# Kernel optimization log

Hardware: AMD Instinct MI355X
Metric: run time of the kernel (lower is better)

The kernel has to match this reference:

```python
import jax, jax.numpy as jnp
import numpy as np

D_MODEL = 1024
NUM_HEADS = 16
HEAD_DIM = D_MODEL // NUM_HEADS


def setup_inputs() -> dict:
    key = jax.random.key(0)
    ks = jax.random.split(key, 5)
    x = jax.random.normal(ks[0], (4, 2048, D_MODEL), dtype=jnp.float32)
    # nn.Linear params: weight [out, in], bias [out]
    s_qkv = 1.0 / np.sqrt(D_MODEL)
    W_qkv = jax.random.uniform(ks[1], (3 * D_MODEL, D_MODEL), jnp.float32, -s_qkv, s_qkv)
    b_qkv = jax.random.uniform(ks[2], (3 * D_MODEL,), jnp.float32, -s_qkv, s_qkv)
    W_proj = jax.random.uniform(ks[3], (D_MODEL, D_MODEL), jnp.float32, -s_qkv, s_qkv)
    b_proj = jax.random.uniform(ks[4], (D_MODEL,), jnp.float32, -s_qkv, s_qkv)
    return {"x": x, "W_qkv": W_qkv, "b_qkv": b_qkv, "W_proj": W_proj, "b_proj": b_proj}


def reference(x, W_qkv, b_qkv, W_proj, b_proj):
    B, S, D = x.shape
    H, Hd = NUM_HEADS, HEAD_DIM
    qkv = x @ W_qkv.T + b_qkv                      # [B,S,3D]
    qkv = qkv.reshape(B, S, 3, H, Hd)
    q = qkv[:, :, 0].transpose(0, 2, 1, 3)        # [B,H,S,Hd]
    k = qkv[:, :, 1].transpose(0, 2, 1, 3)
    v = qkv[:, :, 2].transpose(0, 2, 1, 3)
    scale = jnp.sqrt(jnp.asarray(Hd, x.dtype))
    attn = jnp.einsum('bhqd,bhkd->bhqk', q, k) / scale   # [B,H,S,S]
    attn = jax.nn.softmax(attn, axis=-1)
    out = jnp.einsum('bhqk,bhkd->bhqd', attn, v)         # [B,H,S,Hd]
    out = out.transpose(0, 2, 1, 3).reshape(B, S, D)
    return out @ W_proj.T + b_proj
```

## Files before the change

### kernel.cpp

```cpp
#include <hip/hip_runtime.h>
#include <stdint.h>

#define SEQ    2048
#define DMODEL 1024
#define NH     16
#define HD     64
#define BATCH  4
#define MTOT   (BATCH*SEQ)
#define NT2    (SEQ/128)

typedef __attribute__((ext_vector_type(8))) short bf16x8;
typedef __attribute__((ext_vector_type(4))) float f32x4;
typedef __attribute__((ext_vector_type(2))) unsigned int uint2v;

#define QSCALE (0.125f * 1.44269504088896f)

__device__ __forceinline__ unsigned short f2bf(float f) {
  union { float f; uint32_t u; } x; x.f = f;
  uint32_t u = x.u;
  u += 0x7FFFu + ((u >> 16) & 1u);
  return (unsigned short)(u >> 16);
}

__device__ __forceinline__ float exp2_fast(float x) {
#if __has_builtin(__builtin_amdgcn_exp2f)
  return __builtin_amdgcn_exp2f(x);
#else
  return __expf(x * 0.69314718056f);
#endif
}

__device__ __forceinline__ uint32_t cvt_pk_bf16(float lo, float hi) {
  uint32_t r;
  asm("v_cvt_pk_bf16_f32 %0, %1, %2" : "=v"(r) : "v"(lo), "v"(hi));
  return r;
}

__device__ __forceinline__ void swap32(uint32_t& x, uint32_t& y) {
#if __has_builtin(__builtin_amdgcn_permlane32_swap)
  uint2v r = __builtin_amdgcn_permlane32_swap(x, y, false, false);
  x = r[0]; y = r[1];
#else
  unsigned int xs = __shfl_xor((unsigned int)x, 32);
  unsigned int ys = __shfl_xor((unsigned int)y, 32);
  const bool lo = ((threadIdx.x & 63) & 32) == 0;
  x = lo ? x : (uint32_t)ys;
  y = lo ? (uint32_t)xs : y;
#endif
}

__device__ __forceinline__ void swap16(uint32_t& x, uint32_t& y) {
#if __has_builtin(__builtin_amdgcn_permlane16_swap)
  uint2v r = __builtin_amdgcn_permlane16_swap(x, y, false, false);
  x = r[0]; y = r[1];
#else
  unsigned int xs = __shfl_xor((unsigned int)x, 16);
  unsigned int ys = __shfl_xor((unsigned int)y, 16);
  const bool lo = ((threadIdx.x & 63) & 16) == 0;
  x = lo ? x : (uint32_t)ys;
  y = lo ? (uint32_t)xs : y;
#endif
}

__device__ __forceinline__ void gload_lds16(const ushort* g, ushort* l) {
  __builtin_amdgcn_global_load_lds(
      (const __attribute__((address_space(1))) uint32_t*)g,
      (__attribute__((address_space(3))) uint32_t*)l, 16, 0, 0);
}

__global__ __launch_bounds__(256) void cvt_kernel(const float* __restrict__ in,
                                                  ushort* __restrict__ out, int n4) {
  int i = blockIdx.x * 256 + threadIdx.x;
  if (i >= n4) return;
  float4 v = ((const float4*)in)[i];
  ushort4 o;
  o.x = f2bf(v.x); o.y = f2bf(v.y); o.z = f2bf(v.z); o.w = f2bf(v.w);
  ((ushort4*)out)[i] = o;
}

template<int MODE>
__global__ __launch_bounds__(256)
void gemm_nt(const ushort* __restrict__ A, const ushort* __restrict__ B,
             const float* __restrict__ bias, float* __restrict__ outf,
             ushort* __restrict__ qo, ushort* __restrict__ ko, ushort* __restrict__ vto,
             int M, int N, int K)
{
  __shared__ ushort lda[128 * 64];
  __shared__ ushort ldb[128 * 64];
  const int tid = threadIdx.x;
  const int w = tid >> 6, lane = tid & 63;
  const int l15 = lane & 15, lg = lane >> 4;

  const int Nb = gridDim.x, Mb = gridDim.y;
  const int flat = blockIdx.y * Nb + blockIdx.x;
  const int q8 = (Nb * Mb) >> 3;
  const int nf2 = (flat & 7) * q8 + (flat >> 3);
  const int row0 = (nf2 % Mb) * 128;
  const int col0 = (nf2 / Mb) * 128;

  const int wm = (w >> 1) * 64, wn = (w & 1) * 64;
  const int sr = lane >> 3;
  const int scb = (lane & 7) ^ sr;
  const int rswz = l15 & 7;

  f32x4 acc[4][4];
#pragma unroll
  for (int i = 0; i < 4; ++i)
#pragma unroll
    for (int j = 0; j < 4; ++j) acc[i][j] = (f32x4){0.f, 0.f, 0.f, 0.f};

  const ushort* Ablk = A + (size_t)row0 * K;
  const ushort* Bblk = B + (size_t)col0 * K;

  for (int kt = 0; kt < K; kt += 64) {
#pragma unroll
    for (int i = 0; i < 4; ++i) {
      const int is = w * 4 + i;
      gload_lds16(Ablk + (size_t)(is * 8 + sr) * K + kt + scb * 8, lda + is * 512);
      gload_lds16(Bblk + (size_t)(is * 8 + sr) * K + kt + scb * 8, ldb + is * 512);
    }
    __syncthreads();
#pragma unroll
    for (int kki = 0; kki < 2; ++kki) {
      bf16x8 af[4], bfr[4];
#pragma unroll
      for (int i = 0; i < 4; ++i)
        af[i] = *(const bf16x8*)&lda[(wm + i * 16 + l15) * 64 + ((kki * 4 + lg) ^ rswz) * 8];
#pragma unroll
      for (int j = 0; j < 4; ++j)
        bfr[j] = *(const bf16x8*)&ldb[(wn + j * 16 + l15) * 64 + ((kki * 4 + lg) ^ rswz) * 8];
#pragma unroll
      for (int i = 0; i < 4; ++i)
#pragma unroll
        for (int j = 0; j < 4; ++j)
          acc[i][j] = __builtin_amdgcn_mfma_f32_16x16x32_bf16(af[i], bfr[j], acc[i][j], 0, 0, 0);
    }
    __syncthreads();
  }

#pragma unroll
  for (int i = 0; i < 4; ++i)
#pragma unroll
    for (int j = 0; j < 4; ++j) {
      const int n = col0 + wn + j * 16 + l15;
      const int m0 = row0 + wm + i * 16 + lg * 4;
      const float bn = bias[n];
      if (MODE == 1) {
#pragma unroll
        for (int r = 0; r < 4; ++r)
          outf[(size_t)(m0 + r) * N + n] = acc[i][j][r] + bn;
      } else {
        const int d = n & 1023;
        const int hh = d >> 6, hd = d & 63;
        const int bb = m0 >> 11, ss0 = m0 & 2047;
        const int which = n >> 10;
        if (which == 2) {
          ushort4 pk;
          pk.x = f2bf(acc[i][j][0] + bn);
          pk.y = f2bf(acc[i][j][1] + bn);
          pk.z = f2bf(acc[i][j][2] + bn);
          pk.w = f2bf(acc[i][j][3] + bn);
          *(ushort4*)&vto[(((size_t)bb * NH + hh) * HD + hd) * SEQ + ss0] = pk;
        } else {
          const size_t idx = (((size_t)bb * NH + hh) * SEQ + ss0) * HD + hd;
#pragma unroll
          for (int r = 0; r < 4; ++r) {
            const float val = acc[i][j][r] + bn;
            if (which == 0) qo[idx + (size_t)r * HD] = f2bf(val * QSCALE);
            else            ko[idx + (size_t)r * HD] = f2bf(val);
          }
        }
      }
    }
}

__global__ __launch_bounds__(256, 2)
void attn_kernel(const ushort* __restrict__ Q, const ushort* __restrict__ Kg,
                 const ushort* __restrict__ Vtg, ushort* __restrict__ O)
{
  __shared__ ushort ldk[2][2][64 * 64];
  __shared__ ushort ldvt[2][2][64 * 64];

  const int tid = threadIdx.x;
  const int w = tid >> 6, lane = tid & 63;
  const int l15 = lane & 15, lg = lane >> 4;

  const int bid = blockIdx.x;
  const int c = bid & 7, j = bid >> 3;
  const int bh = c + 8 * (j >> 3);
  const int qt = j & 7;
  const int b = bh >> 4, h = bh & 15;

  const ushort* Qb = Q + (size_t)bh * SEQ * HD;
  const ushort* Kb = Kg + (size_t)bh * SEQ * HD;
  const ushort* Vtb = Vtg + (size_t)bh * HD * SEQ;

  const int srow = lane >> 3;
  const int scb = (lane & 7) ^ srow;
  const int rswz = l15 & 7;

  const int qr0 = qt * 256 + w * 64;
  bf16x8 qf[4][2];
#pragma unroll
  for (int mi = 0; mi < 4; ++mi)
#pragma unroll
    for (int dk = 0; dk < 2; ++dk)
      qf[mi][dk] = *(const bf16x8*)&Qb[(size_t)(qr0 + mi * 16 + l15) * HD + dk * 32 + lg * 8];

  bf16x8 ones;
#pragma unroll
  for (int i = 0; i < 8; ++i) ones[i] = (short)0x3F80;

  f32x4 acc_o[4][4];
  f32x4 acc_l[4];
#pragma unroll
  for (int mi = 0; mi < 4; ++mi) {
#pragma unroll
    for (int nf = 0; nf < 4; ++nf) acc_o[mi][nf] = (f32x4){0.f, 0.f, 0.f, 0.f};
    acc_l[mi] = (f32x4){0.f, 0.f, 0.f, 0.f};
  }

#define STAGE(bufi, grp) do {                                                                  \
    _Pragma("unroll")                                                                          \
    for (int s_ = 0; s_ < 2; ++s_) {                                                           \
      const int t_ = 2 * (grp) + s_;                                                           \
      const ushort* Ks_ = Kb + (size_t)t_ * 64 * HD;                                           \
      const ushort* Vs_ = Vtb + (size_t)t_ * 64;                                               \
      _Pragma("unroll")                                                                        \
      for (int i_ = 0; i_ < 2; ++i_) {                                                         \
        const int is_ = w * 2 + i_;                                                            \
        gload_lds16(Ks_ + (size_t)(is_ * 8 + srow) * HD + scb * 8, &ldk[bufi][s_][is_ * 512]); \
        gload_lds16(Vs_ + (size_t)(is_ * 8 + srow) * SEQ + scb * 8, &ldvt[bufi][s_][is_ * 512]);\
      }                                                                                        \
    }                                                                                          \
  } while (0)

  int cur = 0;
  STAGE(0, 0);
  __syncthreads();

  for (int g = 0; g < NT2; ++g) {
    if (g + 1 < NT2) STAGE(cur ^ 1, g + 1);

#pragma unroll
    for (int s = 0; s < 2; ++s) {
      f32x4 accs[4][4];
#pragma unroll
      for (int a = 0; a < 4; ++a)
#pragma unroll
        for (int mi = 0; mi < 4; ++mi) accs[a][mi] = (f32x4){0.f, 0.f, 0.f, 0.f};
#pragma unroll
      for (int dk = 0; dk < 2; ++dk) {
        bf16x8 kfr[4];
#pragma unroll
        for (int a = 0; a < 4; ++a)
          kfr[a] = *(const bf16x8*)&ldk[cur][s][(a * 16 + l15) * 64 + ((dk * 4 + lg) ^ rswz) * 8];
        __builtin_amdgcn_s_setprio(1);
#pragma unroll
        for (int a = 0; a < 4; ++a)
#pragma unroll
          for (int mi = 0; mi < 4; ++mi)
            accs[a][mi] = __builtin_amdgcn_mfma_f32_16x16x32_bf16(kfr[a], qf[mi][dk], accs[a][mi], 0, 0, 0);
        __builtin_amdgcn_s_setprio(0);
      }

#pragma unroll
      for (int mi = 0; mi < 4; ++mi)
#pragma unroll
        for (int a = 0; a < 4; ++a)
#pragma unroll
          for (int r = 0; r < 4; ++r)
            accs[a][mi][r] = exp2_fast(accs[a][mi][r]);

#pragma unroll
      for (int kk = 0; kk < 2; ++kk) {
        bf16x8 vv[4];
#pragma unroll
        for (int nf = 0; nf < 4; ++nf)
          vv[nf] = *(const bf16x8*)&ldvt[cur][s][(nf * 16 + l15) * 64 + ((kk * 4 + lg) ^ rswz) * 8];
#pragma unroll
        for (int mi = 0; mi < 4; ++mi) {
          uint32_t a0 = cvt_pk_bf16(accs[2 * kk][mi][0], accs[2 * kk][mi][1]);
          uint32_t a1 = cvt_pk_bf16(accs[2 * kk][mi][2], accs[2 * kk][mi][3]);
          uint32_t b0 = cvt_pk_bf16(accs[2 * kk + 1][mi][0], accs[2 * kk + 1][mi][1]);
          uint32_t b1 = cvt_pk_bf16(accs[2 * kk + 1][mi][2], accs[2 * kk + 1][mi][3]);
          swap32(a0, b0); swap32(a1, b1);
          swap16(a0, b0); swap16(a1, b1);
          union { uint32_t d[4]; bf16x8 v; } pu;
          pu.d[0] = a0; pu.d[1] = a1; pu.d[2] = b0; pu.d[3] = b1;
          __builtin_amdgcn_s_setprio(1);
#pragma unroll
          for (int nf = 0; nf < 4; ++nf)
            acc_o[mi][nf] = __builtin_amdgcn_mfma_f32_16x16x32_bf16(vv[nf], pu.v, acc_o[mi][nf], 0, 0, 0);
          acc_l[mi] = __builtin_amdgcn_mfma_f32_16x16x32_bf16(ones, pu.v, acc_l[mi], 0, 0, 0);
          __builtin_amdgcn_s_setprio(0);
        }
      }
    }

    __syncthreads();
    cur ^= 1;
  }
#undef STAGE

#pragma unroll
  for (int mi = 0; mi < 4; ++mi) {
    const float rl = 1.0f / acc_l[mi][0];
    const int row = b * SEQ + qr0 + mi * 16 + l15;
#pragma unroll
    for (int nf = 0; nf < 4; ++nf) {
      ushort4 pk;
      pk.x = f2bf(acc_o[mi][nf][0] * rl);
      pk.y = f2bf(acc_o[mi][nf][1] * rl);
      pk.z = f2bf(acc_o[mi][nf][2] * rl);
      pk.w = f2bf(acc_o[mi][nf][3] * rl);
      *(ushort4*)&O[(size_t)row * DMODEL + h * HD + nf * 16 + lg * 4] = pk;
    }
  }
}

extern "C" void kernel_launch(void* const* d_in, const int* in_sizes, int n_in,
                              void* d_out, int out_size, void* d_ws, size_t ws_size,
                              hipStream_t stream) {
  const float* x     = (const float*)d_in[0];
  const float* Wqkv  = (const float*)d_in[1];
  const float* bqkv  = (const float*)d_in[2];
  const float* Wproj = (const float*)d_in[3];
  const float* bproj = (const float*)d_in[4];
  float* out = (float*)d_out;

  char* ws = (char*)d_ws;
  ushort* x_bf     = (ushort*)ws;
  ushort* ao       = x_bf;
  ushort* wqkv_bf  = (ushort*)(ws + (16u << 20));
  ushort* wproj_bf = (ushort*)(ws + (22u << 20));
  ushort* q        = (ushort*)(ws + (24u << 20));
  ushort* k        = (ushort*)(ws + (40u << 20));
  ushort* vt       = (ushort*)(ws + (56u << 20));

  cvt_kernel<<<(MTOT * DMODEL / 4) / 256, 256, 0, stream>>>(x, x_bf, MTOT * DMODEL / 4);
  cvt_kernel<<<(3 * DMODEL * DMODEL / 4) / 256, 256, 0, stream>>>(Wqkv, wqkv_bf, 3 * DMODEL * DMODEL / 4);
  cvt_kernel<<<(DMODEL * DMODEL / 4) / 256, 256, 0, stream>>>(Wproj, wproj_bf, DMODEL * DMODEL / 4);

  gemm_nt<0><<<dim3(3 * DMODEL / 128, MTOT / 128), 256, 0, stream>>>(
      x_bf, wqkv_bf, bqkv, nullptr, q, k, vt, MTOT, 3 * DMODEL, DMODEL);

  attn_kernel<<<dim3(512), 256, 0, stream>>>(q, k, vt, ao);

  gemm_nt<1><<<dim3(DMODEL / 128, MTOT / 128), 256, 0, stream>>>(
      ao, wproj_bf, bproj, out, nullptr, nullptr, nullptr, MTOT, DMODEL, DMODEL);
}
```

Before: 186.0 us.

## Double-buffer GEMM LDS tiles and merge three conversion launches into one

The GEMM main loop now uses two LDS buffers per operand and issues the global-to-LDS loads for the next K tile before computing on the current one. This lets load latency overlap with MFMA work and drops one barrier per iteration. The three fp32-to-bf16 conversion kernels are merged into one launch that dispatches on the flat index, removing two launch gaps. In exchange, LDS use doubles to 64KB per block, which may cut occupancy.

```diff
diff --git a/kernel.cpp b/kernel.cpp
--- a/kernel.cpp
+++ b/kernel.cpp
@@ -68,14 +68,20 @@
       (__attribute__((address_space(3))) uint32_t*)l, 16, 0, 0);
 }
 
-__global__ __launch_bounds__(256) void cvt_kernel(const float* __restrict__ in,
-                                                  ushort* __restrict__ out, int n4) {
+__global__ __launch_bounds__(256) void cvt3_kernel(
+    const float* __restrict__ a, ushort* __restrict__ oa, int na4,
+    const float* __restrict__ b, ushort* __restrict__ ob, int nb4,
+    const float* __restrict__ c, ushort* __restrict__ oc, int nc4) {
   int i = blockIdx.x * 256 + threadIdx.x;
-  if (i >= n4) return;
-  float4 v = ((const float4*)in)[i];
+  const float* src; ushort* dst; int idx;
+  if (i < na4)              { src = a; dst = oa; idx = i; }
+  else if (i < na4 + nb4)   { src = b; dst = ob; idx = i - na4; }
+  else if (i < na4 + nb4 + nc4) { src = c; dst = oc; idx = i - na4 - nb4; }
+  else return;
+  float4 v = ((const float4*)src)[idx];
   ushort4 o;
   o.x = f2bf(v.x); o.y = f2bf(v.y); o.z = f2bf(v.z); o.w = f2bf(v.w);
-  ((ushort4*)out)[i] = o;
+  ((ushort4*)dst)[idx] = o;
 }
 
 template<int MODE>
@@ -85,8 +91,8 @@
              ushort* __restrict__ qo, ushort* __restrict__ ko, ushort* __restrict__ vto,
              int M, int N, int K)
 {
-  __shared__ ushort lda[128 * 64];
-  __shared__ ushort ldb[128 * 64];
+  __shared__ ushort lda[2][128 * 64];
+  __shared__ ushort ldb[2][128 * 64];
   const int tid = threadIdx.x;
   const int w = tid >> 6, lane = tid & 63;
   const int l15 = lane & 15, lg = lane >> 4;
@@ -112,23 +118,31 @@
   const ushort* Ablk = A + (size_t)row0 * K;
   const ushort* Bblk = B + (size_t)col0 * K;
 
+#define GSTAGE(buf, ktv) do {                                                              \
+    _Pragma("unroll")                                                                      \
+    for (int i_ = 0; i_ < 4; ++i_) {                                                       \
+      const int is_ = w * 4 + i_;                                                          \
+      gload_lds16(Ablk + (size_t)(is_ * 8 + sr) * K + (ktv) + scb * 8, &lda[buf][is_ * 512]); \
+      gload_lds16(Bblk + (size_t)(is_ * 8 + sr) * K + (ktv) + scb * 8, &ldb[buf][is_ * 512]); \
+    }                                                                                      \
+  } while (0)
+
+  int cur = 0;
+  GSTAGE(0, 0);
+  __syncthreads();
+
   for (int kt = 0; kt < K; kt += 64) {
-#pragma unroll
-    for (int i = 0; i < 4; ++i) {
-      const int is = w * 4 + i;
-      gload_lds16(Ablk + (size_t)(is * 8 + sr) * K + kt + scb * 8, lda + is * 512);
-      gload_lds16(Bblk + (size_t)(is * 8 + sr) * K + kt + scb * 8, ldb + is * 512);
-    }
-    __syncthreads();
+    if (kt + 64 < K) GSTAGE(cur ^ 1, kt + 64);
+
 #pragma unroll
     for (int kki = 0; kki < 2; ++kki) {
       bf16x8 af[4], bfr[4];
 #pragma unroll
       for (int i = 0; i < 4; ++i)
-        af[i] = *(const bf16x8*)&lda[(wm + i * 16 + l15) * 64 + ((kki * 4 + lg) ^ rswz) * 8];
+        af[i] = *(const bf16x8*)&lda[cur][(wm + i * 16 + l15) * 64 + ((kki * 4 + lg) ^ rswz) * 8];
 #pragma unroll
       for (int j = 0; j < 4; ++j)
-        bfr[j] = *(const bf16x8*)&ldb[(wn + j * 16 + l15) * 64 + ((kki * 4 + lg) ^ rswz) * 8];
+        bfr[j] = *(const bf16x8*)&ldb[cur][(wn + j * 16 + l15) * 64 + ((kki * 4 + lg) ^ rswz) * 8];
 #pragma unroll
       for (int i = 0; i < 4; ++i)
 #pragma unroll
@@ -136,7 +150,9 @@
           acc[i][j] = __builtin_amdgcn_mfma_f32_16x16x32_bf16(af[i], bfr[j], acc[i][j], 0, 0, 0);
     }
     __syncthreads();
+    cur ^= 1;
   }
+#undef GSTAGE
 
 #pragma unroll
   for (int i = 0; i < 4; ++i)
@@ -338,9 +354,11 @@
   ushort* k        = (ushort*)(ws + (40u << 20));
   ushort* vt       = (ushort*)(ws + (56u << 20));
 
-  cvt_kernel<<<(MTOT * DMODEL / 4) / 256, 256, 0, stream>>>(x, x_bf, MTOT * DMODEL / 4);
-  cvt_kernel<<<(3 * DMODEL * DMODEL / 4) / 256, 256, 0, stream>>>(Wqkv, wqkv_bf, 3 * DMODEL * DMODEL / 4);
-  cvt_kernel<<<(DMODEL * DMODEL / 4) / 256, 256, 0, stream>>>(Wproj, wproj_bf, DMODEL * DMODEL / 4);
+  const int na4 = MTOT * DMODEL / 4;
+  const int nb4 = 3 * DMODEL * DMODEL / 4;
+  const int nc4 = DMODEL * DMODEL / 4;
+  cvt3_kernel<<<(na4 + nb4 + nc4 + 255) / 256, 256, 0, stream>>>(
+      x, x_bf, na4, Wqkv, wqkv_bf, nb4, Wproj, wproj_bf, nc4);
 
   gemm_nt<0><<<dim3(3 * DMODEL / 128, MTOT / 128), 256, 0, stream>>>(
       x_bf, wqkv_bf, bqkv, nullptr, q, k, vt, MTOT, 3 * DMODEL, DMODEL);
```

New measurement: 186.1 us. About the same (+0.0%).
